# Kernel optimization log

Measured on AMD Instinct MI355X. Metric: run time of the kernel, lower is better.

Reference implementation:

```python
import jax, jax.numpy as jnp
import numpy as np

A, H, HI = 4, 3, 2  # nagents, n_pol_heads, n_intr_rew_heads (sep_extr_head=True)
# leave-one-out index table: row i lists all agents k != i, in ascending order (torch loop order)
LOO = np.array([[k for k in range(A) if k != i] for i in range(A)])  # [A, A-1]


def setup_inputs() -> dict:
    key = jax.random.key(0)
    ks = jax.random.split(key, 12)
    B, S, C, D = 32768, 256, 16, 128  # batch, vect_state_size, action_size, hidden_dim
    IN = C * (A - 1) + D  # 176 critic input dim
    r = lambda k, shp, s=0.05: jax.random.normal(k, shp, dtype=jnp.float32) * s
    return {
        "state_vect": jax.random.normal(ks[0], (B, S), dtype=jnp.float32),
        "acs": jax.random.normal(ks[1], (A, H, B, C), dtype=jnp.float32),
        "enc_W": r(ks[2], (S, D)),
        "enc_b": r(ks[3], (D,)),
        "extr_W1": r(ks[4], (H, A, IN, D)),
        "extr_b1": r(ks[5], (H, A, D)),
        "extr_W2": r(ks[6], (H, A, D, C)),
        "extr_b2": r(ks[7], (H, A, C)),
        "intr_W1": r(ks[8], (HI, A, IN, D)),
        "intr_b1": r(ks[9], (HI, A, D)),
        "intr_W2": r(ks[10], (HI, A, D, C)),
        "intr_b2": r(ks[11], (HI, A, C)),
    }


def reference(state_vect, acs, enc_W, enc_b, extr_W1, extr_b1, extr_W2, extr_b2,
              intr_W1, intr_b1, intr_W2, intr_b2):
    B, C = acs.shape[2], acs.shape[3]
    D = enc_W.shape[1]
    # shared state encoder: Linear -> ReLU
    enc = jax.nn.relu(state_vect @ enc_W + enc_b)  # [B, D]
    # leave-one-out action concat per (agent, head): cat(acs[k!=i, j]) ++ enc
    rel = acs[LOO]                                 # [A, A-1, H, B, C]
    rel = rel.transpose(0, 2, 3, 1, 4).reshape(A, H, B, (A - 1) * C)
    x = jnp.concatenate([rel, jnp.broadcast_to(enc, (A, H, B, D))], axis=-1)  # [A,H,B,IN]
    # greedy action index of agent i's own head-j policy output
    int_acs = jnp.argmax(acs, axis=-1)             # [A, H, B]

    def critic(xin, W1, b1, W2, b2):
        # xin: [A, Hc, B, IN]; W1: [Hc, A, IN, D]; W2: [Hc, A, D, C]
        h = jax.nn.relu(jnp.einsum('ahbi,haid->ahbd', xin, W1)
                        + b1.transpose(1, 0, 2)[:, :, None, :])
        return (jnp.einsum('ahbd,hadc->ahbc', h, W2)
                + b2.transpose(1, 0, 2)[:, :, None, :])  # [A, Hc, B, C]

    extr_all_q = critic(x, extr_W1, extr_b1, extr_W2, extr_b2)          # [A,H,B,C]
    extr_q = jnp.take_along_axis(extr_all_q, int_acs[..., None], axis=-1)  # [A,H,B,1]
    # intr critics exist only for heads j>=1 (sep_extr_head=True -> offset -1)
    intr_all_q = critic(x[:, 1:], intr_W1, intr_b1, intr_W2, intr_b2)   # [A,HI,B,C]
    intr_q = jnp.take_along_axis(intr_all_q, int_acs[:, 1:, :, None], axis=-1)  # [A,HI,B,1]
    return extr_q, intr_q
```

## Files before the change

### kernel.cpp

```cpp
#include <hip/hip_runtime.h>

#define NA 4
#define NH 3
#define NHI 2
#define Bsz 32768
#define Ssz 256
#define Csz 16
#define Dsz 128
#define INsz 176
#define NP 20
#define KP 192

typedef __bf16 v8bf __attribute__((ext_vector_type(8)));
typedef float v4f __attribute__((ext_vector_type(4)));

#define OFF_ENC    0
#define OFF_ACSBF  8388608
#define OFF_W1F    20971520
#define OFF_ENCWF  21954560
#define OFF_W2T    22020096
#define OFF_AMX    22102016
#define OFF_ZERO   22495232

#define N_ACSROW (NA*NH*Bsz)
#define N_W1F   (NP*192*32)
#define N_ENCWF (256*32)
#define N_W2T   (NP*Csz*Dsz)
#define N_ZERO  16
#define N_PREP  (N_ACSROW+N_W1F+N_ENCWF+N_W2T+N_ZERO)

__global__ __launch_bounds__(256) void prep_kernel(
    const float* __restrict__ acs, const float* __restrict__ encW,
    const float* __restrict__ eW1, const float* __restrict__ iW1,
    const float* __restrict__ eW2, const float* __restrict__ iW2,
    char* __restrict__ ws)
{
    long tid = (long)blockIdx.x * 256 + threadIdx.x;

    if (tid < N_ACSROW) {
        const float4* src = (const float4*)(acs + (size_t)tid * 16);
        float4 f0 = src[0], f1 = src[1], f2 = src[2], f3 = src[3];
        float v[16] = {f0.x,f0.y,f0.z,f0.w, f1.x,f1.y,f1.z,f1.w,
                       f2.x,f2.y,f2.z,f2.w, f3.x,f3.y,f3.z,f3.w};
        v8bf o0, o1;
        #pragma unroll
        for (int i = 0; i < 8; ++i) { o0[i] = (__bf16)v[i]; o1[i] = (__bf16)v[8 + i]; }
        v8bf* dst = (v8bf*)(ws + OFF_ACSBF) + tid * 2;
        dst[0] = o0; dst[1] = o1;
        float best = v[0]; int bi = 0;
        #pragma unroll
        for (int c = 1; c < 16; ++c) if (v[c] > best) { best = v[c]; bi = c; }
        ((unsigned char*)(ws + OFF_AMX))[tid] = (unsigned char)bi;
        return;
    }
    tid -= N_ACSROW;
    if (tid < N_W1F) {
        const int n4 = (int)(tid & 31) * 4;
        const int k  = (int)((tid >> 5) % 192);
        const int p  = (int)(tid / 6144);
        const float* W1;
        if (p < 12) { int ai = p / 3, hj = p % 3; W1 = eW1 + (size_t)(hj * NA + ai) * INsz * Dsz; }
        else { int qq = p - 12; int ai = qq >> 1, jj = qq & 1; W1 = iW1 + (size_t)(jj * NA + ai) * INsz * Dsz; }
        float4 f = (k < INsz) ? *(const float4*)(W1 + (size_t)k * Dsz + n4)
                              : (float4){0.f, 0.f, 0.f, 0.f};
        const int kc = k >> 5, q = (k >> 3) & 3, j = k & 7;
        __bf16* dst = (__bf16*)(ws + OFF_W1F);
        const float fv[4] = {f.x, f.y, f.z, f.w};
        #pragma unroll
        for (int i = 0; i < 4; ++i) {
            const int n = n4 + i, nt = n >> 4, m = n & 15;
            dst[((size_t)(p * 6 + kc) * 8 + nt) * 512 + (q * 16 + m) * 8 + j] = (__bf16)fv[i];
        }
        return;
    }
    tid -= N_W1F;
    if (tid < N_ENCWF) {
        const int n4 = (int)(tid & 31) * 4;
        const int k  = (int)(tid >> 5);
        float4 f = *(const float4*)(encW + (size_t)k * Dsz + n4);
        const int kc = k >> 5, q = (k >> 3) & 3, j = k & 7;
        __bf16* dst = (__bf16*)(ws + OFF_ENCWF);
        const float fv[4] = {f.x, f.y, f.z, f.w};
        #pragma unroll
        for (int i = 0; i < 4; ++i) {
            const int n = n4 + i, nt = n >> 4, m = n & 15;
            dst[((size_t)kc * 8 + nt) * 512 + (q * 16 + m) * 8 + j] = (__bf16)fv[i];
        }
        return;
    }
    tid -= N_ENCWF;
    if (tid < N_W2T) {
        int d = (int)(tid & 127);
        int rest = (int)(tid >> 7);
        int c = rest & 15, p = rest >> 4;
        const float* W2;
        if (p < 12) { int ai = p / 3, hj = p % 3; W2 = eW2 + (size_t)(hj * NA + ai) * Dsz * Csz; }
        else { int qq = p - 12; int ai = qq >> 1, jj = qq & 1; W2 = iW2 + (size_t)(jj * NA + ai) * Dsz * Csz; }
        ((__bf16*)(ws + OFF_W2T))[(size_t)p * Csz * Dsz + (size_t)c * Dsz + d] = (__bf16)W2[(size_t)d * Csz + c];
        return;
    }
    tid -= N_W2T;
    if (tid < N_ZERO) ((float*)(ws + OFF_ZERO))[tid] = 0.f;
}

__global__ __launch_bounds__(256) void enc_kernel(const float* __restrict__ sv,
                                                  const float* __restrict__ encb,
                                                  char* __restrict__ ws)
{
    const int t = threadIdx.x;
    const int wv = t >> 6, lane = t & 63, m = lane & 15, q = lane >> 4;
    const int R = blockIdx.x * 64 + wv * 16 + m;
    const __bf16* encwf = (const __bf16*)(ws + OFF_ENCWF);
    __bf16* enc = (__bf16*)(ws + OFF_ENC);

    v4f acc[8];
    #pragma unroll
    for (int nt = 0; nt < 8; ++nt) acc[nt] = (v4f){0.f, 0.f, 0.f, 0.f};

    const float* arow = sv + (size_t)R * Ssz + q * 8;
    #pragma unroll
    for (int kc = 0; kc < 8; ++kc) {
        float4 f0 = *(const float4*)(arow + kc * 32);
        float4 f1 = *(const float4*)(arow + kc * 32 + 4);
        v8bf af;
        af[0]=(__bf16)f0.x; af[1]=(__bf16)f0.y; af[2]=(__bf16)f0.z; af[3]=(__bf16)f0.w;
        af[4]=(__bf16)f1.x; af[5]=(__bf16)f1.y; af[6]=(__bf16)f1.z; af[7]=(__bf16)f1.w;
        #pragma unroll
        for (int nt = 0; nt < 8; ++nt) {
            v8bf bf = *(const v8bf*)(encwf + ((size_t)kc * 8 + nt) * 512 + lane * 8);
            acc[nt] = __builtin_amdgcn_mfma_f32_16x16x32_bf16(af, bf, acc[nt], 0, 0, 0);
        }
    }
    const int rbase = blockIdx.x * 64 + wv * 16 + q * 4;
    #pragma unroll
    for (int nt = 0; nt < 8; ++nt) {
        const float bias = encb[nt * 16 + m];
        #pragma unroll
        for (int rg = 0; rg < 4; ++rg) {
            float v = acc[nt][rg] + bias;
            v = v > 0.f ? v : 0.f;
            enc[(size_t)(rbase + rg) * Dsz + nt * 16 + m] = (__bf16)v;
        }
    }
}

__global__ __launch_bounds__(256, 3) void critic_kernel(
    const float* __restrict__ eb1, const float* __restrict__ eb2,
    const float* __restrict__ ib1, const float* __restrict__ ib2,
    const char* __restrict__ ws, float* __restrict__ out)
{
    __shared__ __bf16 w1s[6 * 8 * 512];

    const int t = threadIdx.x;
    const int p  = blockIdx.y;
    const int rb = blockIdx.x;
    const int wv = t >> 6, lane = t & 63, m = lane & 15, q = lane >> 4;
    const int rw = rb * 128 + wv * 32;

    int ai, hj;
    const float *b1, *b2;
    float* outp;
    if (p < 12) {
        ai = p / 3; hj = p % 3;
        const int wi = hj * NA + ai;
        b1 = eb1 + (size_t)wi * Dsz; b2 = eb2 + (size_t)wi * Csz;
        outp = out + (size_t)(ai * NH + hj) * Bsz;
    } else {
        const int qq = p - 12; ai = qq >> 1; const int jj = qq & 1; hj = jj + 1;
        const int wi = jj * NA + ai;
        b1 = ib1 + (size_t)wi * Dsz; b2 = ib2 + (size_t)wi * Csz;
        outp = out + (size_t)NA * NH * Bsz + (size_t)(ai * NHI + jj) * Bsz;
    }

    const __bf16* acsb = (const __bf16*)(ws + OFF_ACSBF);
    const __bf16* encp = (const __bf16*)(ws + OFF_ENC);
    const __bf16* w1f  = (const __bf16*)(ws + OFF_W1F) + (size_t)p * 6 * 8 * 512;
    const __bf16* w2t  = (const __bf16*)(ws + OFF_W2T) + (size_t)p * Csz * Dsz;
    const unsigned char* amx = (const unsigned char*)(ws + OFF_AMX) + (size_t)(ai * NH + hj) * Bsz + rw;
    const __bf16* zerop = (const __bf16*)(ws + OFF_ZERO);

    {
        const v8bf* src = (const v8bf*)w1f;
        v8bf* dst = (v8bf*)w1s;
        #pragma unroll
        for (int i = 0; i < 12; ++i)
            dst[i * 256 + t] = src[i * 256 + t];
    }

    const int loo0 = 0 + (0 >= ai), loo1 = 1 + (1 >= ai), loo2 = 2 + (2 >= ai);
    const __bf16* a0p = acsb + (size_t)(loo0 * NH + hj) * Bsz * Csz;
    const __bf16* a1p = acsb + (size_t)(loo1 * NH + hj) * Bsz * Csz;
    const __bf16* a2p = acsb + (size_t)(loo2 * NH + hj) * Bsz * Csz;

    const int R0 = rw + m;
    const __bf16* base[6];
    int strd[6];
    base[0] = (q < 2) ? (a0p + (size_t)R0 * Csz + q * 8) : (a1p + (size_t)R0 * Csz + (q - 2) * 8);
    strd[0] = Csz;
    base[1] = (q < 2) ? (a2p + (size_t)R0 * Csz + q * 8) : (encp + (size_t)R0 * Dsz + (q - 2) * 8);
    strd[1] = (q < 2) ? Csz : Dsz;
    base[2] = encp + (size_t)R0 * Dsz + 16 + q * 8;  strd[2] = Dsz;
    base[3] = encp + (size_t)R0 * Dsz + 48 + q * 8;  strd[3] = Dsz;
    base[4] = encp + (size_t)R0 * Dsz + 80 + q * 8;  strd[4] = Dsz;
    base[5] = (q < 2) ? (encp + (size_t)R0 * Dsz + 112 + q * 8) : zerop;
    strd[5] = (q < 2) ? Dsz : 0;

    v4f acc[2][8];
    #pragma unroll
    for (int i = 0; i < 2; ++i)
        #pragma unroll
        for (int j = 0; j < 8; ++j)
            acc[i][j] = (v4f){0.f, 0.f, 0.f, 0.f};

    __syncthreads();

    #pragma unroll
    for (int kc = 0; kc < 6; ++kc) {
        v8bf af[2];
        #pragma unroll
        for (int mt = 0; mt < 2; ++mt)
            af[mt] = *(const v8bf*)(base[kc] + (size_t)(mt * 16) * strd[kc]);
        #pragma unroll
        for (int nt = 0; nt < 8; ++nt) {
            v8bf bf = *(const v8bf*)&w1s[((size_t)kc * 8 + nt) * 512 + lane * 8];
            acc[0][nt] = __builtin_amdgcn_mfma_f32_16x16x32_bf16(af[0], bf, acc[0][nt], 0, 0, 0);
            acc[1][nt] = __builtin_amdgcn_mfma_f32_16x16x32_bf16(af[1], bf, acc[1][nt], 0, 0, 0);
        }
    }

    float b1v[8];
    #pragma unroll
    for (int nt = 0; nt < 8; ++nt) b1v[nt] = b1[nt * 16 + m];

    #pragma unroll
    for (int mt = 0; mt < 2; ++mt) {
        const int rowb = mt * 16 + q * 4;
        const unsigned int cw = *(const unsigned int*)(amx + rowb);
        #pragma unroll
        for (int rg = 0; rg < 4; ++rg) {
            const int c = (cw >> (8 * rg)) & 255;
            const __bf16* wc = w2t + (size_t)c * Dsz + m;
            float partial = 0.f;
            #pragma unroll
            for (int nt = 0; nt < 8; ++nt) {
                float h = acc[mt][nt][rg] + b1v[nt];
                h = h > 0.f ? h : 0.f;
                partial += h * (float)wc[nt * 16];
            }
            partial += __shfl_xor(partial, 1, 64);
            partial += __shfl_xor(partial, 2, 64);
            partial += __shfl_xor(partial, 4, 64);
            partial += __shfl_xor(partial, 8, 64);
            if (m == 0)
                outp[rw + rowb + rg] = partial + b2[c];
        }
    }
}

extern "C" void kernel_launch(void* const* d_in, const int* in_sizes, int n_in,
                              void* d_out, int out_size, void* d_ws, size_t ws_size,
                              hipStream_t stream) {
    const float* sv   = (const float*)d_in[0];
    const float* acs  = (const float*)d_in[1];
    const float* encW = (const float*)d_in[2];
    const float* encb = (const float*)d_in[3];
    const float* eW1  = (const float*)d_in[4];
    const float* eb1  = (const float*)d_in[5];
    const float* eW2  = (const float*)d_in[6];
    const float* eb2  = (const float*)d_in[7];
    const float* iW1  = (const float*)d_in[8];
    const float* ib1  = (const float*)d_in[9];
    const float* iW2  = (const float*)d_in[10];
    const float* ib2  = (const float*)d_in[11];
    float* out = (float*)d_out;
    char* ws = (char*)d_ws;

    hipLaunchKernelGGL(prep_kernel, dim3((N_PREP + 255) / 256), dim3(256), 0, stream,
                       acs, encW, eW1, iW1, eW2, iW2, ws);
    hipLaunchKernelGGL(enc_kernel, dim3(Bsz / 64), dim3(256), 0, stream, sv, encb, ws);
    hipLaunchKernelGGL(critic_kernel, dim3(Bsz / 128, NP), dim3(256), 0, stream,
                       eb1, eb2, ib1, ib2, ws, out);
}
```

Before: 178.8 us.

## Merge prep and encoder kernels; double critic row tile per wave

Fuses the encoder GEMM into the prep kernel by giving separate block ranges to encoding and preprocessing. Each encoder block converts enc_W to the bf16 fragment layout in shared memory itself, which removes one launch and the global staging of that weight. The critic kernel now covers 256 rows per block, 64 per wave with 4 M-tiles, so each shared W1 fragment is reused more. Occupancy drops to 2 blocks per CU, more registers are used, and the grid is half as large. Encoder blocks also repeat the strided enc_W conversion redundantly.

```diff
diff --git a/kernel.cpp b/kernel.cpp
--- a/kernel.cpp
+++ b/kernel.cpp
@@ -17,25 +17,83 @@
 #define OFF_ENC    0
 #define OFF_ACSBF  8388608
 #define OFF_W1F    20971520
-#define OFF_ENCWF  21954560
 #define OFF_W2T    22020096
 #define OFF_AMX    22102016
 #define OFF_ZERO   22495232
 
 #define N_ACSROW (NA*NH*Bsz)
 #define N_W1F   (NP*192*32)
-#define N_ENCWF (256*32)
 #define N_W2T   (NP*Csz*Dsz)
 #define N_ZERO  16
-#define N_PREP  (N_ACSROW+N_W1F+N_ENCWF+N_W2T+N_ZERO)
-
-__global__ __launch_bounds__(256) void prep_kernel(
+#define N_PREP  (N_ACSROW+N_W1F+N_W2T+N_ZERO)
+#define ENC_BLOCKS (Bsz / 64)
+#define PREP_BLOCKS ((N_PREP + 255) / 256)
+
+__global__ __launch_bounds__(256) void pe_kernel(
+    const float* __restrict__ sv, const float* __restrict__ encb,
     const float* __restrict__ acs, const float* __restrict__ encW,
     const float* __restrict__ eW1, const float* __restrict__ iW1,
     const float* __restrict__ eW2, const float* __restrict__ iW2,
     char* __restrict__ ws)
 {
-    long tid = (long)blockIdx.x * 256 + threadIdx.x;
+    __shared__ __bf16 encs[8 * 8 * 512];
+    const int t = threadIdx.x;
+
+    if (blockIdx.x < ENC_BLOCKS) {
+        #pragma unroll
+        for (int i = 0; i < 16; ++i) {
+            const int slot = i * 256 + t;
+            const int kcnt = slot >> 6;
+            const int ln   = slot & 63;
+            const int kc = kcnt >> 3, nt = kcnt & 7;
+            const int qq = ln >> 4, mm = ln & 15;
+            const int krow = kc * 32 + qq * 8;
+            const int col  = nt * 16 + mm;
+            v8bf o;
+            #pragma unroll
+            for (int j = 0; j < 8; ++j)
+                o[j] = (__bf16)encW[(size_t)(krow + j) * Dsz + col];
+            *(v8bf*)&encs[(size_t)kcnt * 512 + ln * 8] = o;
+        }
+        __syncthreads();
+
+        const int wv = t >> 6, lane = t & 63, m = lane & 15, q = lane >> 4;
+        const int R = blockIdx.x * 64 + wv * 16 + m;
+        __bf16* enc = (__bf16*)(ws + OFF_ENC);
+
+        v4f acc[8];
+        #pragma unroll
+        for (int nt = 0; nt < 8; ++nt) acc[nt] = (v4f){0.f, 0.f, 0.f, 0.f};
+
+        const float* arow = sv + (size_t)R * Ssz + q * 8;
+        #pragma unroll
+        for (int kc = 0; kc < 8; ++kc) {
+            float4 f0 = *(const float4*)(arow + kc * 32);
+            float4 f1 = *(const float4*)(arow + kc * 32 + 4);
+            v8bf af;
+            af[0]=(__bf16)f0.x; af[1]=(__bf16)f0.y; af[2]=(__bf16)f0.z; af[3]=(__bf16)f0.w;
+            af[4]=(__bf16)f1.x; af[5]=(__bf16)f1.y; af[6]=(__bf16)f1.z; af[7]=(__bf16)f1.w;
+            #pragma unroll
+            for (int nt = 0; nt < 8; ++nt) {
+                v8bf bf = *(const v8bf*)&encs[((size_t)kc * 8 + nt) * 512 + lane * 8];
+                acc[nt] = __builtin_amdgcn_mfma_f32_16x16x32_bf16(af, bf, acc[nt], 0, 0, 0);
+            }
+        }
+        const int rbase = blockIdx.x * 64 + wv * 16 + q * 4;
+        #pragma unroll
+        for (int nt = 0; nt < 8; ++nt) {
+            const float bias = encb[nt * 16 + m];
+            #pragma unroll
+            for (int rg = 0; rg < 4; ++rg) {
+                float v = acc[nt][rg] + bias;
+                v = v > 0.f ? v : 0.f;
+                enc[(size_t)(rbase + rg) * Dsz + nt * 16 + m] = (__bf16)v;
+            }
+        }
+        return;
+    }
+
+    long tid = (long)(blockIdx.x - ENC_BLOCKS) * 256 + t;
 
     if (tid < N_ACSROW) {
         const float4* src = (const float4*)(acs + (size_t)tid * 16);
@@ -74,21 +132,6 @@
         return;
     }
     tid -= N_W1F;
-    if (tid < N_ENCWF) {
-        const int n4 = (int)(tid & 31) * 4;
-        const int k  = (int)(tid >> 5);
-        float4 f = *(const float4*)(encW + (size_t)k * Dsz + n4);
-        const int kc = k >> 5, q = (k >> 3) & 3, j = k & 7;
-        __bf16* dst = (__bf16*)(ws + OFF_ENCWF);
-        const float fv[4] = {f.x, f.y, f.z, f.w};
-        #pragma unroll
-        for (int i = 0; i < 4; ++i) {
-            const int n = n4 + i, nt = n >> 4, m = n & 15;
-            dst[((size_t)kc * 8 + nt) * 512 + (q * 16 + m) * 8 + j] = (__bf16)fv[i];
-        }
-        return;
-    }
-    tid -= N_ENCWF;
     if (tid < N_W2T) {
         int d = (int)(tid & 127);
         int rest = (int)(tid >> 7);
@@ -103,48 +146,7 @@
     if (tid < N_ZERO) ((float*)(ws + OFF_ZERO))[tid] = 0.f;
 }
 
-__global__ __launch_bounds__(256) void enc_kernel(const float* __restrict__ sv,
-                                                  const float* __restrict__ encb,
-                                                  char* __restrict__ ws)
-{
-    const int t = threadIdx.x;
-    const int wv = t >> 6, lane = t & 63, m = lane & 15, q = lane >> 4;
-    const int R = blockIdx.x * 64 + wv * 16 + m;
-    const __bf16* encwf = (const __bf16*)(ws + OFF_ENCWF);
-    __bf16* enc = (__bf16*)(ws + OFF_ENC);
-
-    v4f acc[8];
-    #pragma unroll
-    for (int nt = 0; nt < 8; ++nt) acc[nt] = (v4f){0.f, 0.f, 0.f, 0.f};
-
-    const float* arow = sv + (size_t)R * Ssz + q * 8;
-    #pragma unroll
-    for (int kc = 0; kc < 8; ++kc) {
-        float4 f0 = *(const float4*)(arow + kc * 32);
-        float4 f1 = *(const float4*)(arow + kc * 32 + 4);
-        v8bf af;
-        af[0]=(__bf16)f0.x; af[1]=(__bf16)f0.y; af[2]=(__bf16)f0.z; af[3]=(__bf16)f0.w;
-        af[4]=(__bf16)f1.x; af[5]=(__bf16)f1.y; af[6]=(__bf16)f1.z; af[7]=(__bf16)f1.w;
-        #pragma unroll
-        for (int nt = 0; nt < 8; ++nt) {
-            v8bf bf = *(const v8bf*)(encwf + ((size_t)kc * 8 + nt) * 512 + lane * 8);
-            acc[nt] = __builtin_amdgcn_mfma_f32_16x16x32_bf16(af, bf, acc[nt], 0, 0, 0);
-        }
-    }
-    const int rbase = blockIdx.x * 64 + wv * 16 + q * 4;
-    #pragma unroll
-    for (int nt = 0; nt < 8; ++nt) {
-        const float bias = encb[nt * 16 + m];
-        #pragma unroll
-        for (int rg = 0; rg < 4; ++rg) {
-            float v = acc[nt][rg] + bias;
-            v = v > 0.f ? v : 0.f;
-            enc[(size_t)(rbase + rg) * Dsz + nt * 16 + m] = (__bf16)v;
-        }
-    }
-}
-
-__global__ __launch_bounds__(256, 3) void critic_kernel(
+__global__ __launch_bounds__(256, 2) void critic_kernel(
     const float* __restrict__ eb1, const float* __restrict__ eb2,
     const float* __restrict__ ib1, const float* __restrict__ ib2,
     const char* __restrict__ ws, float* __restrict__ out)
@@ -155,7 +157,7 @@
     const int p  = blockIdx.y;
     const int rb = blockIdx.x;
     const int wv = t >> 6, lane = t & 63, m = lane & 15, q = lane >> 4;
-    const int rw = rb * 128 + wv * 32;
+    const int rw = rb * 256 + wv * 64;
 
     int ai, hj;
     const float *b1, *b2;
@@ -205,9 +207,9 @@
     base[5] = (q < 2) ? (encp + (size_t)R0 * Dsz + 112 + q * 8) : zerop;
     strd[5] = (q < 2) ? Dsz : 0;
 
-    v4f acc[2][8];
-    #pragma unroll
-    for (int i = 0; i < 2; ++i)
+    v4f acc[4][8];
+    #pragma unroll
+    for (int i = 0; i < 4; ++i)
         #pragma unroll
         for (int j = 0; j < 8; ++j)
             acc[i][j] = (v4f){0.f, 0.f, 0.f, 0.f};
@@ -216,15 +218,16 @@
 
     #pragma unroll
     for (int kc = 0; kc < 6; ++kc) {
-        v8bf af[2];
-        #pragma unroll
-        for (int mt = 0; mt < 2; ++mt)
+        v8bf af[4];
+        #pragma unroll
+        for (int mt = 0; mt < 4; ++mt)
             af[mt] = *(const v8bf*)(base[kc] + (size_t)(mt * 16) * strd[kc]);
         #pragma unroll
         for (int nt = 0; nt < 8; ++nt) {
             v8bf bf = *(const v8bf*)&w1s[((size_t)kc * 8 + nt) * 512 + lane * 8];
-            acc[0][nt] = __builtin_amdgcn_mfma_f32_16x16x32_bf16(af[0], bf, acc[0][nt], 0, 0, 0);
-            acc[1][nt] = __builtin_amdgcn_mfma_f32_16x16x32_bf16(af[1], bf, acc[1][nt], 0, 0, 0);
+            #pragma unroll
+            for (int mt = 0; mt < 4; ++mt)
+                acc[mt][nt] = __builtin_amdgcn_mfma_f32_16x16x32_bf16(af[mt], bf, acc[mt][nt], 0, 0, 0);
         }
     }
 
@@ -233,7 +236,7 @@
     for (int nt = 0; nt < 8; ++nt) b1v[nt] = b1[nt * 16 + m];
 
     #pragma unroll
-    for (int mt = 0; mt < 2; ++mt) {
+    for (int mt = 0; mt < 4; ++mt) {
         const int rowb = mt * 16 + q * 4;
         const unsigned int cw = *(const unsigned int*)(amx + rowb);
         #pragma unroll
@@ -275,9 +278,8 @@
     float* out = (float*)d_out;
     char* ws = (char*)d_ws;
 
-    hipLaunchKernelGGL(prep_kernel, dim3((N_PREP + 255) / 256), dim3(256), 0, stream,
-                       acs, encW, eW1, iW1, eW2, iW2, ws);
-    hipLaunchKernelGGL(enc_kernel, dim3(Bsz / 64), dim3(256), 0, stream, sv, encb, ws);
-    hipLaunchKernelGGL(critic_kernel, dim3(Bsz / 128, NP), dim3(256), 0, stream,
+    hipLaunchKernelGGL(pe_kernel, dim3(ENC_BLOCKS + PREP_BLOCKS), dim3(256), 0, stream,
+                       sv, encb, acs, encW, eW1, iW1, eW2, iW2, ws);
+    hipLaunchKernelGGL(critic_kernel, dim3(Bsz / 256, NP), dim3(256), 0, stream,
                        eb1, eb2, ib1, ib2, ws, out);
 }
```

Result: slower. 183.9 us (+2.9%).
